# Performance work log

Measured on AMD Instinct MI355X. Metric: run time of the kernel, lower is better.

Reference implementation:

```python
import jax, jax.numpy as jnp
import numpy as np

H = 8
DQ = 32
DK = 32
DV = 32
DC = DQ + DK  # concat dim for additive attention


def setup_inputs() -> dict:
    key = jax.random.key(0)
    ks = jax.random.split(key, 8)
    bs, Lq, Lk = 2, 384, 384
    q = jax.random.normal(ks[0], (bs, Lq, H * DQ), jnp.float32)
    k = jax.random.normal(ks[1], (bs, Lk, H * DK), jnp.float32)
    v = jax.random.normal(ks[2], (bs, Lk, H * DV), jnp.float32)
    q_sequence_lengths = jax.random.randint(ks[3], (bs,), 1, Lq + 1, dtype=jnp.int32)
    k_sequence_lengths = jax.random.randint(ks[4], (bs,), 1, Lk + 1, dtype=jnp.int32)
    bound = 1.0 / np.sqrt(DC)
    w1 = jax.random.uniform(ks[5], (H, DC, DC), jnp.float32, -bound, bound)
    b1 = jax.random.uniform(ks[6], (H, DC), jnp.float32, -bound, bound)
    w2 = jax.random.uniform(ks[7], (H, DC), jnp.float32, -1.0, 1.0)
    return {"q": q, "k": k, "v": v,
            "q_sequence_lengths": q_sequence_lengths,
            "k_sequence_lengths": k_sequence_lengths,
            "w1": w1, "b1": b1, "w2": w2}


def reference(q, k, v, q_sequence_lengths, k_sequence_lengths, w1, b1, w2):
    bs, Lq, _ = q.shape
    Lk = k.shape[1]
    # split heads: (b, h, L, d)
    qh = q.reshape(bs, Lq, H, DQ).transpose(0, 2, 1, 3)
    kh = k.reshape(bs, Lk, H, DK).transpose(0, 2, 1, 3)
    vh = v.reshape(bs, Lk, H, DV).transpose(0, 2, 1, 3)
    # additive scores: tanh(cat(q_i, k_j) @ W1 + b1) @ w2
    # cat @ W1 == q @ W1[:DQ] + k @ W1[DQ:]  (avoids materializing the cat)
    qW = jnp.einsum('bhqd,hde->bhqe', qh, w1[:, :DQ, :])
    kW = jnp.einsum('bhkd,hde->bhke', kh, w1[:, DQ:, :])
    hid = jnp.tanh(qW[:, :, :, None, :] + kW[:, :, None, :, :] + b1[None, :, None, None, :])  # (b,h,q,k,DC)
    scores = jnp.einsum('bhqke,he->bhqk', hid, w2)
    # key-side length mask (end padded)
    kmask = jnp.arange(Lk)[None, :] < k_sequence_lengths[:, None]  # (b, Lk)
    scores = jnp.where(kmask[:, None, None, :], scores, jnp.float32(-1e9))
    att = jax.nn.softmax(scores, axis=-1)  # (b,h,q,k)
    out = jnp.einsum('bhqk,bhkd->bqhd', att, vh)  # (b,q,h,DV)
    # query-side length mask zeros out padded query rows
    qmask = jnp.arange(Lq)[None, :] < q_sequence_lengths[:, None]  # (b, Lq)
    out = out * qmask[:, :, None, None].astype(out.dtype)
    return out.reshape(bs, Lq, H * DV), att
```

## Files before the change

kernel.cpp:

```cpp
#include <hip/hip_runtime.h>

#define NH 8
#define LQ 384
#define LK 384
#define BS 2

typedef float v2f __attribute__((ext_vector_type(2)));
__device__ __forceinline__ v2f fma2(v2f a, v2f b, v2f c) { return __builtin_elementwise_fma(a, b, c); }
__device__ __forceinline__ v2f sp(float x) { v2f r; r.x = x; r.y = x; return r; }

__global__ __launch_bounds__(256) void pre_ek_kernel(
    const float* __restrict__ kin, const float* __restrict__ w1,
    const float* __restrict__ b1, float* __restrict__ ws)
{
    __shared__ float tile[32][65];
    const int bid = blockIdx.x;
    const int bh = bid / 12, kt = bid % 12;
    const int b = bh >> 3, h = bh & 7;
    const int k0 = kt * 32;
    const int lane = threadIdx.x & 63, w = threadIdx.x >> 6;

    float w1c[32];
    const float* w1p = w1 + (size_t)(h * 64 + 32) * 64 + lane;
    #pragma unroll
    for (int d = 0; d < 32; ++d) w1c[d] = w1p[d * 64];
    const float bv = b1[h * 64 + lane];

    #pragma unroll
    for (int s = 0; s < 8; ++s) {
        int kr = w * 8 + s;
        const float* krow = kin + ((size_t)(b * LK + k0 + kr)) * (NH * 32) + h * 32;
        float acc = bv;
        #pragma unroll
        for (int d = 0; d < 32; ++d) acc = __builtin_fmaf(krow[d], w1c[d], acc);
        tile[kr][lane] = __expf(acc + acc);
    }
    __syncthreads();
    #pragma unroll
    for (int r = 0; r < 2; ++r) {
        int f = threadIdx.x + r * 256;
        int e4 = f >> 5, k32 = f & 31;
        float4 o;
        o.x = tile[k32][e4 * 4 + 0];
        o.y = tile[k32][e4 * 4 + 1];
        o.z = tile[k32][e4 * 4 + 2];
        o.w = tile[k32][e4 * 4 + 3];
        ((float4*)ws)[((size_t)(bh * 16 + e4)) * LK + k0 + k32] = o;
    }
}

__global__ __launch_bounds__(256) void attn_kernel(
    const float* __restrict__ qin, const float* __restrict__ vin,
    const int* __restrict__ qlens, const int* __restrict__ klens,
    const float* __restrict__ w1, const float* __restrict__ w2g,
    const float* __restrict__ ws,
    float* __restrict__ outg, float* __restrict__ attg)
{
    __shared__ __align__(16) float eqi_s[2][128];
    __shared__ __align__(16) float att_h[4][2 * 192];
    __shared__ __align__(16) float w2s[64];
    __shared__ float2 smu[2][2][2];
    __shared__ __align__(16) float4 pvp[2][2][2][8];

    const int tid = threadIdx.x, wave = tid >> 6, lane = tid & 63;
    const int pair = wave >> 1, hh = wave & 1;
    const int bh = blockIdx.x / 96, tile = blockIdx.x % 96;
    const int b = bh >> 3, h = bh & 7;
    const int q0 = tile * 4;
    const int klen = klens[b], qlen = qlens[b];

    {
        const float* w1p = w1 + (size_t)h * 64 * 64 + lane;
        const float* qp  = qin + ((size_t)(b * LQ + q0 + wave)) * (NH * 32) + h * 32;
        float a = 0.f;
        #pragma unroll
        for (int d = 0; d < 32; ++d) a = __builtin_fmaf(qp[d], w1p[d * 64], a);
        eqi_s[pair][lane * 2 + hh] = __expf(a + a);
        if (wave == 0) w2s[lane] = w2g[h * 64 + lane];
    }
    __syncthreads();

    v2f sc[3];
    sc[0] = sp(0.f); sc[1] = sp(0.f); sc[2] = sp(0.f);
    const float4* ekq = (const float4*)ws + ((size_t)bh * 16) * LK + hh * 192 + lane;
    const v2f*   eqp = (const v2f*)eqi_s[pair];
    const float4* w2p = (const float4*)w2s;

    float4 kv[3];
    #pragma unroll
    for (int c = 0; c < 3; ++c) kv[c] = ekq[c * 64];

    #pragma unroll
    for (int e4 = 0; e4 < 16; ++e4) {
        float4 nkv[3];
        if (e4 < 15) {
            const float4* np = ekq + (size_t)(e4 + 1) * LK;
            #pragma unroll
            for (int c = 0; c < 3; ++c) nkv[c] = np[c * 64];
        }
        v2f E0 = eqp[e4 * 4 + 0];
        v2f E1 = eqp[e4 * 4 + 1];
        v2f E2 = eqp[e4 * 4 + 2];
        v2f E3 = eqp[e4 * 4 + 3];
        float4 wv = w2p[e4];
        #pragma unroll
        for (int c = 0; c < 3; ++c) {
            float4 kq = kv[c];
            v2f t0 = fma2(E0, sp(kq.x), sp(1.f));
            v2f t1 = fma2(E1, sp(kq.y), sp(1.f));
            v2f t2 = fma2(E2, sp(kq.z), sp(1.f));
            v2f t3 = fma2(E3, sp(kq.w), sp(1.f));
            v2f p12 = t0 * t1, p34 = t2 * t3;
            v2f n12 = fma2(sp(wv.y), t0, sp(wv.x) * t1);
            v2f n34 = fma2(sp(wv.w), t2, sp(wv.z) * t3);
            v2f num = fma2(n34, p12, n12 * p34);
            v2f den = p12 * p34;
            v2f r;
            r.x = __builtin_amdgcn_rcpf(den.x);
            r.y = __builtin_amdgcn_rcpf(den.y);
            sc[c] = fma2(num, r, sc[c]);
        }
        if (e4 < 15) {
            #pragma unroll
            for (int c = 0; c < 3; ++c) kv[c] = nkv[c];
        }
    }

    float s0_[3], s1_[3];
    float m0 = -3.4e38f, m1 = -3.4e38f;
    #pragma unroll
    for (int c = 0; c < 3; ++c) {
        int kk = hh * 192 + c * 64 + lane;
        s0_[c] = (kk < klen) ? -2.0f * sc[c].x : -3.4e38f;
        s1_[c] = (kk < klen) ? -2.0f * sc[c].y : -3.4e38f;
        m0 = fmaxf(m0, s0_[c]);
        m1 = fmaxf(m1, s1_[c]);
    }
    #pragma unroll
    for (int off = 32; off >= 1; off >>= 1) {
        m0 = fmaxf(m0, __shfl_xor(m0, off));
        m1 = fmaxf(m1, __shfl_xor(m1, off));
    }
    float e0_[3], e1_[3];
    float u0 = 0.f, u1 = 0.f;
    #pragma unroll
    for (int c = 0; c < 3; ++c) {
        int kk = hh * 192 + c * 64 + lane;
        e0_[c] = (kk < klen) ? __expf(s0_[c] - m0) : 0.f;
        e1_[c] = (kk < klen) ? __expf(s1_[c] - m1) : 0.f;
        u0 += e0_[c];
        u1 += e1_[c];
    }
    #pragma unroll
    for (int off = 32; off >= 1; off >>= 1) {
        u0 += __shfl_xor(u0, off);
        u1 += __shfl_xor(u1, off);
    }
    if (lane == 0) {
        smu[pair][0][hh] = make_float2(m0, u0);
        smu[pair][1][hh] = make_float2(m1, u1);
    }
    __syncthreads();
    float f0, f1;
    {
        float2 a = smu[pair][0][0], c2 = smu[pair][0][1];
        float m = fmaxf(a.x, c2.x);
        float u = a.y * __expf(a.x - m) + c2.y * __expf(c2.x - m);
        f0 = __expf(m0 - m) * __builtin_amdgcn_rcpf(u);
        float2 a1 = smu[pair][1][0], c1 = smu[pair][1][1];
        float m_ = fmaxf(a1.x, c1.x);
        float u_ = a1.y * __expf(a1.x - m_) + c1.y * __expf(c1.x - m_);
        f1 = __expf(m1 - m_) * __builtin_amdgcn_rcpf(u_);
    }

    float p0[3], p1[3];
    {
        float* ar = att_h[wave];
        #pragma unroll
        for (int c = 0; c < 3; ++c) {
            p0[c] = e0_[c] * f0;
            p1[c] = e1_[c] * f1;
            ar[c * 64 + lane]       = p0[c];
            ar[192 + c * 64 + lane] = p1[c];
        }
    }

    const int kf = lane >> 3, dg = lane & 7;
    const float* vbase = vin + (size_t)b * LK * (NH * 32) + h * 32
                       + (size_t)(hh * 192 + kf) * (NH * 32) + dg * 4;
    const float* a0p = att_h[wave];
    const float* a1p = att_h[wave] + 192;
    float oa0[4] = {0.f,0.f,0.f,0.f}, oa1[4] = {0.f,0.f,0.f,0.f};
    #pragma unroll 8
    for (int k0 = 0; k0 < 192; k0 += 8) {
        float4 vv = *(const float4*)(vbase + (size_t)k0 * (NH * 32));
        float a0 = a0p[k0 + kf];
        float a1 = a1p[k0 + kf];
        oa0[0] = __builtin_fmaf(a0, vv.x, oa0[0]);
        oa0[1] = __builtin_fmaf(a0, vv.y, oa0[1]);
        oa0[2] = __builtin_fmaf(a0, vv.z, oa0[2]);
        oa0[3] = __builtin_fmaf(a0, vv.w, oa0[3]);
        oa1[0] = __builtin_fmaf(a1, vv.x, oa1[0]);
        oa1[1] = __builtin_fmaf(a1, vv.y, oa1[1]);
        oa1[2] = __builtin_fmaf(a1, vv.z, oa1[2]);
        oa1[3] = __builtin_fmaf(a1, vv.w, oa1[3]);
    }
    #pragma unroll
    for (int u = 0; u < 4; ++u) {
        oa0[u] += __shfl_xor(oa0[u], 8);
        oa0[u] += __shfl_xor(oa0[u], 16);
        oa0[u] += __shfl_xor(oa0[u], 32);
        oa1[u] += __shfl_xor(oa1[u], 8);
        oa1[u] += __shfl_xor(oa1[u], 16);
        oa1[u] += __shfl_xor(oa1[u], 32);
    }
    if (kf == 0) {
        pvp[pair][hh][0][dg] = make_float4(oa0[0], oa0[1], oa0[2], oa0[3]);
        pvp[pair][hh][1][dg] = make_float4(oa1[0], oa1[1], oa1[2], oa1[3]);
    }
    __syncthreads();

    if (lane < 8) {
        int q = q0 + wave;
        float4 xa = pvp[wave >> 1][0][wave & 1][lane];
        float4 xb = pvp[wave >> 1][1][wave & 1][lane];
        float4 o4;
        bool ok = (q < qlen);
        o4.x = ok ? (xa.x + xb.x) : 0.f;
        o4.y = ok ? (xa.y + xb.y) : 0.f;
        o4.z = ok ? (xa.z + xb.z) : 0.f;
        o4.w = ok ? (xa.w + xb.w) : 0.f;
        ((float4*)(outg + ((size_t)(b * LQ + q)) * (NH * 32) + h * 32))[lane] = o4;
    }

    {
        float* ag = attg + ((size_t)(bh * LQ + q0 + 2 * pair)) * LK + hh * 192;
        #pragma unroll
        for (int c = 0; c < 3; ++c) ag[c * 64 + lane] = p0[c];
        ag += LK;
        #pragma unroll
        for (int c = 0; c < 3; ++c) ag[c * 64 + lane] = p1[c];
    }
}

extern "C" void kernel_launch(void* const* d_in, const int* in_sizes, int n_in,
                              void* d_out, int out_size, void* d_ws, size_t ws_size,
                              hipStream_t stream) {
    const float* q    = (const float*)d_in[0];
    const float* k    = (const float*)d_in[1];
    const float* v    = (const float*)d_in[2];
    const int*   qlen = (const int*)d_in[3];
    const int*   klen = (const int*)d_in[4];
    const float* w1   = (const float*)d_in[5];
    const float* b1   = (const float*)d_in[6];
    const float* w2   = (const float*)d_in[7];
    float* out = (float*)d_out;
    float* att = out + (size_t)BS * LQ * NH * 32;
    float* ws  = (float*)d_ws;

    pre_ek_kernel<<<192, 256, 0, stream>>>(k, w1, b1, ws);
    attn_kernel<<<1536, 256, 0, stream>>>(q, v, qlen, klen, w1, w2, ws, out, att);
}
```

Measured before the change: 98.68 us.

## Defer softmax normalization past PV, double-buffer loads, split pre-kernel finer

The PV accumulation now runs on unnormalized exponentials, and the cross-wave max/sum exchange barrier moves after the PV loop, so the softmax factor is applied to the reduced outputs and the stored attention. This lets the first barrier wait overlap with V loads and FMAs. The score loop prefetches two e4 steps ahead and the V loop keeps a two-deep register buffer. The key-precompute kernel uses 16-row tiles and twice as many blocks to fill more CUs. Register pressure rises with the extra buffers, and more math is recomputed at the end.

```diff
diff --git a/kernel.cpp b/kernel.cpp
--- a/kernel.cpp
+++ b/kernel.cpp
@@ -13,12 +13,13 @@
     const float* __restrict__ kin, const float* __restrict__ w1,
     const float* __restrict__ b1, float* __restrict__ ws)
 {
-    __shared__ float tile[32][65];
+    __shared__ float tile[16][65];
     const int bid = blockIdx.x;
-    const int bh = bid / 12, kt = bid % 12;
+    const int bh = bid / 24, kt = bid % 24;
     const int b = bh >> 3, h = bh & 7;
-    const int k0 = kt * 32;
-    const int lane = threadIdx.x & 63, w = threadIdx.x >> 6;
+    const int k0 = kt * 16;
+    const int tid = threadIdx.x;
+    const int lane = tid & 63, w = tid >> 6;
 
     float w1c[32];
     const float* w1p = w1 + (size_t)(h * 64 + 32) * 64 + lane;
@@ -27,8 +28,8 @@
     const float bv = b1[h * 64 + lane];
 
     #pragma unroll
-    for (int s = 0; s < 8; ++s) {
-        int kr = w * 8 + s;
+    for (int s = 0; s < 4; ++s) {
+        int kr = w * 4 + s;
         const float* krow = kin + ((size_t)(b * LK + k0 + kr)) * (NH * 32) + h * 32;
         float acc = bv;
         #pragma unroll
@@ -36,16 +37,14 @@
         tile[kr][lane] = __expf(acc + acc);
     }
     __syncthreads();
-    #pragma unroll
-    for (int r = 0; r < 2; ++r) {
-        int f = threadIdx.x + r * 256;
-        int e4 = f >> 5, k32 = f & 31;
+    {
+        int e4 = tid >> 4, k16 = tid & 15;
         float4 o;
-        o.x = tile[k32][e4 * 4 + 0];
-        o.y = tile[k32][e4 * 4 + 1];
-        o.z = tile[k32][e4 * 4 + 2];
-        o.w = tile[k32][e4 * 4 + 3];
-        ((float4*)ws)[((size_t)(bh * 16 + e4)) * LK + k0 + k32] = o;
+        o.x = tile[k16][e4 * 4 + 0];
+        o.y = tile[k16][e4 * 4 + 1];
+        o.z = tile[k16][e4 * 4 + 2];
+        o.w = tile[k16][e4 * 4 + 3];
+        ((float4*)ws)[((size_t)(bh * 16 + e4)) * LK + k0 + k16] = o;
     }
 }
 
@@ -86,26 +85,29 @@
     const v2f*   eqp = (const v2f*)eqi_s[pair];
     const float4* w2p = (const float4*)w2s;
 
-    float4 kv[3];
-    #pragma unroll
-    for (int c = 0; c < 3; ++c) kv[c] = ekq[c * 64];
+    float4 kva[3], kvb[3];
+    #pragma unroll
+    for (int c = 0; c < 3; ++c) kva[c] = ekq[c * 64];
+    #pragma unroll
+    for (int c = 0; c < 3; ++c) kvb[c] = ekq[LK + c * 64];
 
     #pragma unroll
     for (int e4 = 0; e4 < 16; ++e4) {
-        float4 nkv[3];
-        if (e4 < 15) {
-            const float4* np = ekq + (size_t)(e4 + 1) * LK;
-            #pragma unroll
-            for (int c = 0; c < 3; ++c) nkv[c] = np[c * 64];
+        float4* cur = (e4 & 1) ? kvb : kva;
+        float4 kq0 = cur[0], kq1 = cur[1], kq2 = cur[2];
+        if (e4 < 14) {
+            const float4* np = ekq + (size_t)(e4 + 2) * LK;
+            cur[0] = np[0]; cur[1] = np[64]; cur[2] = np[128];
         }
         v2f E0 = eqp[e4 * 4 + 0];
         v2f E1 = eqp[e4 * 4 + 1];
         v2f E2 = eqp[e4 * 4 + 2];
         v2f E3 = eqp[e4 * 4 + 3];
         float4 wv = w2p[e4];
+        float4 kqs[3] = {kq0, kq1, kq2};
         #pragma unroll
         for (int c = 0; c < 3; ++c) {
-            float4 kq = kv[c];
+            float4 kq = kqs[c];
             v2f t0 = fma2(E0, sp(kq.x), sp(1.f));
             v2f t1 = fma2(E1, sp(kq.y), sp(1.f));
             v2f t2 = fma2(E2, sp(kq.z), sp(1.f));
@@ -120,10 +122,6 @@
             r.y = __builtin_amdgcn_rcpf(den.y);
             sc[c] = fma2(num, r, sc[c]);
         }
-        if (e4 < 15) {
-            #pragma unroll
-            for (int c = 0; c < 3; ++c) kv[c] = nkv[c];
-        }
     }
 
     float s0_[3], s1_[3];
@@ -160,28 +158,12 @@
         smu[pair][0][hh] = make_float2(m0, u0);
         smu[pair][1][hh] = make_float2(m1, u1);
     }
-    __syncthreads();
-    float f0, f1;
-    {
-        float2 a = smu[pair][0][0], c2 = smu[pair][0][1];
-        float m = fmaxf(a.x, c2.x);
-        float u = a.y * __expf(a.x - m) + c2.y * __expf(c2.x - m);
-        f0 = __expf(m0 - m) * __builtin_amdgcn_rcpf(u);
-        float2 a1 = smu[pair][1][0], c1 = smu[pair][1][1];
-        float m_ = fmaxf(a1.x, c1.x);
-        float u_ = a1.y * __expf(a1.x - m_) + c1.y * __expf(c1.x - m_);
-        f1 = __expf(m1 - m_) * __builtin_amdgcn_rcpf(u_);
-    }
-
-    float p0[3], p1[3];
     {
         float* ar = att_h[wave];
         #pragma unroll
         for (int c = 0; c < 3; ++c) {
-            p0[c] = e0_[c] * f0;
-            p1[c] = e1_[c] * f1;
-            ar[c * 64 + lane]       = p0[c];
-            ar[192 + c * 64 + lane] = p1[c];
+            ar[c * 64 + lane]       = e0_[c];
+            ar[192 + c * 64 + lane] = e1_[c];
         }
     }
 
@@ -191,9 +173,14 @@
     const float* a0p = att_h[wave];
     const float* a1p = att_h[wave] + 192;
     float oa0[4] = {0.f,0.f,0.f,0.f}, oa1[4] = {0.f,0.f,0.f,0.f};
-    #pragma unroll 8
-    for (int k0 = 0; k0 < 192; k0 += 8) {
-        float4 vv = *(const float4*)(vbase + (size_t)k0 * (NH * 32));
+    float4 vbuf[2];
+    vbuf[0] = *(const float4*)(vbase);
+    vbuf[1] = *(const float4*)(vbase + (size_t)8 * (NH * 32));
+    #pragma unroll
+    for (int i = 0; i < 24; ++i) {
+        float4 vv = vbuf[i & 1];
+        if (i < 22) vbuf[i & 1] = *(const float4*)(vbase + (size_t)((i + 2) * 8) * (NH * 32));
+        int k0 = i * 8;
         float a0 = a0p[k0 + kf];
         float a1 = a1p[k0 + kf];
         oa0[0] = __builtin_fmaf(a0, vv.x, oa0[0]);
@@ -214,9 +201,23 @@
         oa1[u] += __shfl_xor(oa1[u], 16);
         oa1[u] += __shfl_xor(oa1[u], 32);
     }
+    __syncthreads();
+
+    float f0, f1;
+    {
+        float2 a = smu[pair][0][0], c2 = smu[pair][0][1];
+        float m = fmaxf(a.x, c2.x);
+        float u = a.y * __expf(a.x - m) + c2.y * __expf(c2.x - m);
+        f0 = __expf(m0 - m) * __builtin_amdgcn_rcpf(u);
+        float2 a1 = smu[pair][1][0], c1 = smu[pair][1][1];
+        float m_ = fmaxf(a1.x, c1.x);
+        float u_ = a1.y * __expf(a1.x - m_) + c1.y * __expf(c1.x - m_);
+        f1 = __expf(m1 - m_) * __builtin_amdgcn_rcpf(u_);
+    }
+
     if (kf == 0) {
-        pvp[pair][hh][0][dg] = make_float4(oa0[0], oa0[1], oa0[2], oa0[3]);
-        pvp[pair][hh][1][dg] = make_float4(oa1[0], oa1[1], oa1[2], oa1[3]);
+        pvp[pair][hh][0][dg] = make_float4(oa0[0] * f0, oa0[1] * f0, oa0[2] * f0, oa0[3] * f0);
+        pvp[pair][hh][1][dg] = make_float4(oa1[0] * f1, oa1[1] * f1, oa1[2] * f1, oa1[3] * f1);
     }
     __syncthreads();
 
@@ -236,10 +237,10 @@
     {
         float* ag = attg + ((size_t)(bh * LQ + q0 + 2 * pair)) * LK + hh * 192;
         #pragma unroll
-        for (int c = 0; c < 3; ++c) ag[c * 64 + lane] = p0[c];
+        for (int c = 0; c < 3; ++c) ag[c * 64 + lane] = e0_[c] * f0;
         ag += LK;
         #pragma unroll
-        for (int c = 0; c < 3; ++c) ag[c * 64 + lane] = p1[c];
+        for (int c = 0; c < 3; ++c) ag[c * 64 + lane] = e1_[c] * f1;
     }
 }
 
@@ -258,6 +259,6 @@
     float* att = out + (size_t)BS * LQ * NH * 32;
     float* ws  = (float*)d_ws;
 
-    pre_ek_kernel<<<192, 256, 0, stream>>>(k, w1, b1, ws);
+    pre_ek_kernel<<<384, 256, 0, stream>>>(k, w1, b1, ws);
     attn_kernel<<<1536, 256, 0, stream>>>(q, v, qlen, klen, w1, w2, ws, out, att);
 }
```

After: 97.69 us. Within noise of the previous version (-1.0%).
